# Optimization experiments

Measured on AMD Instinct MI355X. Metric: run time of the kernel, lower is better.

## Reference

```python
import jax, jax.numpy as jnp
import numpy as np

T = 2048        # q_len (current chunk)
P = 2048        # past KV cache length
HID = 4096      # hidden_size
H = 32          # num_attention_heads
D = HID // H    # head_dim = 128
THETA = 10000.0


def apply_rope(x, pos):
    # x: [H, T, D], pos: [T] int
    half = D // 2
    inv_freq = 1.0 / (THETA ** (jnp.arange(0, half, dtype=jnp.float32) / half))
    ang = pos.astype(jnp.float32)[:, None] * inv_freq[None, :]      # [T, D/2]
    cos = jnp.concatenate([jnp.cos(ang), jnp.cos(ang)], axis=-1)[None]  # [1, T, D]
    sin = jnp.concatenate([jnp.sin(ang), jnp.sin(ang)], axis=-1)[None]
    rot = jnp.concatenate([-x[..., half:], x[..., :half]], axis=-1)
    return x * cos + rot * sin


def setup_inputs() -> dict:
    key = jax.random.key(0)
    ks = jax.random.split(key, 8)
    s = 1.0 / np.sqrt(HID)
    inp = {
        "hidden_states": jax.random.normal(ks[0], (T, HID), dtype=jnp.float32),
        "attention_mask": jnp.triu(jnp.full((T, T), -jnp.inf, dtype=jnp.float32), k=1),
        "Wq": jax.random.normal(ks[1], (HID, HID), dtype=jnp.float32) * s,
        "Wk": jax.random.normal(ks[2], (HID, HID), dtype=jnp.float32) * s,
        "Wv": jax.random.normal(ks[3], (HID, HID), dtype=jnp.float32) * s,
        "Wo": jax.random.normal(ks[4], (HID, HID), dtype=jnp.float32) * s,
        "past_k": jax.random.normal(ks[5], (H, P, D), dtype=jnp.float32),
        "past_v": jax.random.normal(ks[6], (H, P, D), dtype=jnp.float32),
        "position_ids": P + jnp.arange(T, dtype=jnp.int32),
        "past_length": P,
    }
    return inp


def reference(hidden_states, attention_mask, Wq, Wk, Wv, Wo, past_k, past_v,
              position_ids, past_length):
    # QKV projections -> [H, T, D]
    proj = lambda W: (hidden_states @ W).reshape(T, H, D).transpose(1, 0, 2)
    q, k, v = proj(Wq), proj(Wk), proj(Wv)
    q = apply_rope(q, position_ids)
    k = apply_rope(k, position_ids)

    scale = 1.0 / jnp.sqrt(jnp.float32(D))
    # scores against past cache and current chunk (fp32 softmax, as in source)
    past_dots = (jnp.einsum('htd,hsd->hts', q, past_k) * scale).astype(jnp.float32)
    pmask = jnp.where(jnp.arange(P) < past_length, 0.0, -jnp.inf)  # [P]
    past_dots = past_dots + pmask
    cur = ((jnp.einsum('htd,hsd->hts', q, k) * scale) + attention_mask).astype(jnp.float32)

    # online-softmax merge via logsumexp combination
    past_lse = jax.scipy.special.logsumexp(past_dots, axis=-1, keepdims=True)
    cur_lse = jax.scipy.special.logsumexp(cur, axis=-1, keepdims=True)
    tot_lse = jnp.logaddexp(past_lse, cur_lse)
    pw = jnp.exp(past_dots - tot_lse).astype(q.dtype)
    cw = jnp.exp(cur - tot_lse).astype(q.dtype)

    out = jnp.einsum('hts,hsd->htd', pw, past_v) + jnp.einsum('hts,hsd->htd', cw, v)
    out = jnp.where(past_length == 0,
                    jnp.einsum('hts,hsd->htd', jax.nn.softmax(cur, axis=-1).astype(q.dtype), v),
                    out)
    out = out.transpose(1, 0, 2).reshape(T, HID)   # [T, hidden]
    return out @ Wo
```

## Files before the change

kernel.cpp:

```cpp
#include <hip/hip_runtime.h>
#include <cstdint>
#include <cstddef>

#define T_LEN 2048
#define PAST_MAX 2048
#define HID 4096
#define NHEAD 32
#define DHEAD 128

typedef __bf16 bf16_t;
typedef __bf16 bf16x4 __attribute__((ext_vector_type(4)));
typedef __bf16 bf16x8 __attribute__((ext_vector_type(8)));
typedef float  f32x4  __attribute__((ext_vector_type(4)));
typedef float  f32x16 __attribute__((ext_vector_type(16)));
typedef unsigned int u32x4 __attribute__((ext_vector_type(4)));

__device__ __forceinline__ void gload16(const void* g, void* l){
  __builtin_amdgcn_global_load_lds((const __attribute__((address_space(1))) void*)g,
                                   (__attribute__((address_space(3))) void*)l,
                                   16, 0, 0);
}

__device__ __forceinline__ unsigned pack_bf16(float a, float b){
  const unsigned ua = __builtin_bit_cast(unsigned short, (bf16_t)a);
  const unsigned ub = __builtin_bit_cast(unsigned short, (bf16_t)b);
  return ua | (ub << 16);
}

__global__ void cvt2_k(const float* __restrict__ a, bf16_t* __restrict__ ao,
                       const float* __restrict__ b, bf16_t* __restrict__ bo, int n4){
  int i = blockIdx.x * 256 + threadIdx.x;
  if (i < n4){
    const float4 v = ((const float4*)a)[i];
    bf16x4 o = { (bf16_t)v.x, (bf16_t)v.y, (bf16_t)v.z, (bf16_t)v.w };
    ((bf16x4*)ao)[i] = o;
  } else {
    i -= n4;
    const float4 v = ((const float4*)b)[i];
    bf16x4 o = { (bf16_t)v.x, (bf16_t)v.y, (bf16_t)v.z, (bf16_t)v.w };
    ((bf16x4*)bo)[i] = o;
  }
}

__global__ __launch_bounds__(256) void transpose2_k(const float* __restrict__ in,
                                                    bf16_t* __restrict__ out, int R, int C){
  __shared__ float tile[64][65];
  const int r0 = blockIdx.x << 6, c0 = blockIdx.y << 6;
  const size_t bo = (size_t)blockIdx.z * (size_t)R * (size_t)C;
  const int tx = threadIdx.x & 15, ty = threadIdx.x >> 4;
#pragma unroll
  for (int k = 0; k < 4; ++k){
    const float4 v = *(const float4*)(in + bo + (size_t)(r0 + ty + 16*k) * C + c0 + tx*4);
    float* tp = &tile[ty + 16*k][tx*4];
    tp[0] = v.x; tp[1] = v.y; tp[2] = v.z; tp[3] = v.w;
  }
  __syncthreads();
  const int rr0 = (threadIdx.x & 7) * 8;
  const int ccb = threadIdx.x >> 3;
#pragma unroll
  for (int k = 0; k < 2; ++k){
    const int cc = ccb + 32*k;
    bf16x8 o;
#pragma unroll
    for (int j = 0; j < 8; ++j) o[j] = (bf16_t)tile[rr0 + j][cc];
    *(bf16x8*)(out + bo + (size_t)(c0 + cc) * R + r0 + rr0) = o;
  }
}

__global__ __launch_bounds__(256) void transpose3_k(
    const float* __restrict__ s0, const float* __restrict__ s1, const float* __restrict__ s2,
    bf16_t* __restrict__ d0, bf16_t* __restrict__ d1, bf16_t* __restrict__ d2){
  __shared__ float tile[64][65];
  const float* in = (blockIdx.z == 0) ? s0 : (blockIdx.z == 1) ? s1 : s2;
  bf16_t* out = (blockIdx.z == 0) ? d0 : (blockIdx.z == 1) ? d1 : d2;
  const int r0 = blockIdx.x << 6, c0 = blockIdx.y << 6;
  const int tx = threadIdx.x & 15, ty = threadIdx.x >> 4;
#pragma unroll
  for (int k = 0; k < 4; ++k){
    const float4 v = *(const float4*)(in + (size_t)(r0 + ty + 16*k) * HID + c0 + tx*4);
    float* tp = &tile[ty + 16*k][tx*4];
    tp[0] = v.x; tp[1] = v.y; tp[2] = v.z; tp[3] = v.w;
  }
  __syncthreads();
  const int rr0 = (threadIdx.x & 7) * 8;
  const int ccb = threadIdx.x >> 3;
#pragma unroll
  for (int k = 0; k < 2; ++k){
    const int cc = ccb + 32*k;
    bf16x8 o;
#pragma unroll
    for (int j = 0; j < 8; ++j) o[j] = (bf16_t)tile[rr0 + j][cc];
    *(bf16x8*)(out + (size_t)(c0 + cc) * HID + r0 + rr0) = o;
  }
}

__global__ void ropek8_k(bf16_t* __restrict__ K, const int* __restrict__ pos){
  const int idx = blockIdx.x * 256 + threadIdx.x;
  const int jc = idx & 7;
  const int t  = (idx >> 3) & (T_LEN - 1);
  const int h  = idx >> 14;
  const size_t base = ((size_t)h * T_LEN + t) * DHEAD;
  const float p = (float)pos[t];
  bf16x8 lo = *(bf16x8*)(K + base + jc * 8);
  bf16x8 hi = *(bf16x8*)(K + base + 64 + jc * 8);
  bf16x8 olo, ohi;
#pragma unroll
  for (int j = 0; j < 8; ++j){
    const int fi = jc * 8 + j;
    const float invf = __expf(-(float)fi * 0.14391156605212898f);
    float sn, cs;
    sincosf(p * invf, &sn, &cs);
    const float b0 = (float)lo[j], b1 = (float)hi[j];
    olo[j] = (bf16_t)(b0 * cs - b1 * sn);
    ohi[j] = (bf16_t)(b1 * cs + b0 * sn);
  }
  *(bf16x8*)(K + base + jc * 8) = olo;
  *(bf16x8*)(K + base + 64 + jc * 8) = ohi;
}

#define MM6(AF, BF, PR) \
  __builtin_amdgcn_s_setprio(1); \
  _Pragma("unroll") \
  for (int kk = 0; kk < 2; ++kk){ \
    _Pragma("unroll") \
    for (int mf = 0; mf < 4; ++mf){ \
      _Pragma("unroll") \
      for (int ni = 0; ni < 2; ++ni) \
        acc[mf][(PR)*2 + ni] = __builtin_amdgcn_mfma_f32_16x16x32_bf16( \
            AF[mf][kk], BF[ni][kk], acc[mf][(PR)*2 + ni], 0, 0, 0); \
    } \
  } \
  __builtin_amdgcn_s_setprio(0); \
  __builtin_amdgcn_sched_barrier(0);

#define RDA(SET, BUF) \
  _Pragma("unroll") \
  for (int mf = 0; mf < 4; ++mf){ \
    SET[mf][0] = *(const bf16x8*)((BUF) + abase + mf * 2048 + koff0); \
    SET[mf][1] = *(const bf16x8*)((BUF) + abase + mf * 2048 + koff1); \
  }

#define RDB(SET, BUF, UOFF) \
  _Pragma("unroll") \
  for (int ni = 0; ni < 2; ++ni){ \
    SET[ni][0] = *(const bf16x8*)((BUF) + (UOFF) + bbase + ni * 2048 + koff0); \
    SET[ni][1] = *(const bf16x8*)((BUF) + (UOFF) + bbase + ni * 2048 + koff1); \
  }

#define PTOP8 \
  asm volatile("s_waitcnt vmcnt(8)" ::: "memory"); \
  __builtin_amdgcn_s_barrier(); \
  __builtin_amdgcn_sched_barrier(0);

#define PTOP0 \
  asm volatile("s_waitcnt vmcnt(0)" ::: "memory"); \
  __builtin_amdgcn_s_barrier(); \
  __builtin_amdgcn_sched_barrier(0);

#define LGK(N) \
  __builtin_amdgcn_sched_barrier(0); \
  asm volatile("s_waitcnt lgkmcnt(" #N ")" ::: "memory"); \
  __builtin_amdgcn_sched_barrier(0);

__global__ __launch_bounds__(512, 1) void gemmqkv6p_k(
    const bf16_t* __restrict__ A,
    const bf16_t* __restrict__ Bc,
    bf16_t* __restrict__ OQ, bf16_t* __restrict__ OK2, bf16_t* __restrict__ OVT)
{
  const int bid = blockIdx.x;
  const int wg  = (bid & 7) * 64 + (bid >> 3);
  const int mt  = wg & 15;
  const int nt  = wg >> 4;
  const int m0  = mt << 7;
  const int n0g = nt * 384;

  const int tid = threadIdx.x;
  const int wv = tid >> 6, lane = tid & 63, lm = lane & 15, g = lane >> 4;
  const int wr = wv >> 2, wc = wv & 3;

  __shared__ __align__(16) char smem[131072];
  char* const buf0 = smem;
  char* const buf1 = smem + 65536;

  const f32x4 fzero = {0.f, 0.f, 0.f, 0.f};
  f32x4 acc[4][6];
#pragma unroll
  for (int i = 0; i < 4; ++i)
#pragma unroll
    for (int j = 0; j < 6; ++j) acc[i][j] = fzero;

  size_t aoff[2], boff[2];
#pragma unroll
  for (int i = 0; i < 2; ++i){
    const int c = i * 512 + tid;
    const int u = c >> 3;
    const int j = ((c & 7) ^ (u & 7)) << 3;
    aoff[i] = (size_t)(m0 + u) * HID + j;
    const int bcol = (u >> 5) * 96 + (u & 31);
    boff[i] = (size_t)(n0g + bcol) * HID + j;
  }
  const int ldst0 = (wv * 64) << 4;
  const int ldst1 = (512 + wv * 64) << 4;

  auto stgA = [&](char* buf, int kt){
    if ((unsigned)kt < 64u){
      const bf16_t* src = A + (size_t)kt * 64;
      gload16(src + aoff[0], buf + ldst0);
      gload16(src + aoff[1], buf + ldst1);
    }
  };
  auto stgB = [&](char* buf, int kt, int pr){
    if ((unsigned)kt < 64u){
      const bf16_t* src = Bc + (size_t)kt * 64 + (size_t)pr * (32 * HID);
      char* dst = buf + 16384 + pr * 16384;
      gload16(src + boff[0], dst + ldst0);
      gload16(src + boff[1], dst + ldst1);
    }
  };

  const int koff0 = ((0 + g) ^ (lm & 7)) << 4;
  const int koff1 = ((4 + g) ^ (lm & 7)) << 4;
  const int abase = ((wr << 6) + lm) << 7;
  const int bbase = ((wc << 5) + lm) << 7;

  stgA(buf0, 0); stgB(buf0, 0, 0); stgB(buf0, 0, 1); stgB(buf0, 0, 2);
  stgA(buf1, 1); stgB(buf1, 1, 0); stgB(buf1, 1, 1);
  asm volatile("s_waitcnt vmcnt(6)" ::: "memory");
  __builtin_amdgcn_s_barrier();

  bf16x8 afA[4][2], afB[4][2], bU[2][2], bV[2][2];
  RDA(afA, buf0)
  RDB(bU, buf0, 16384)

  for (int i = 0; i < 31; ++i){
    const int kt0 = 2 * i;
    PTOP8
    RDB(bV, buf0, 32768)
    stgB(buf1, kt0 + 1, 2);
    LGK(4)
    MM6(afA, bU, 0)
    PTOP8
    RDB(bU, buf0, 49152)
    stgA(buf0, kt0 + 2); stgB(buf0, kt0 + 2, 0);
    LGK(4)
    MM6(afA, bV, 1)
    PTOP8
    RDA(afB, buf1)
    RDB(bV, buf1, 16384)
    stgB(buf0, kt0 + 2, 1);
    LGK(12)
    MM6(afA, bU, 2)
    PTOP8
    RDB(bU, buf1, 32768)
    stgB(buf0, kt0 + 2, 2);
    LGK(4)
    MM6(afB, bV, 0)
    PTOP8
    RDB(bV, buf1, 49152)
    stgA(buf1, kt0 + 3); stgB(buf1, kt0 + 3, 0);
    LGK(4)
    MM6(afB, bU, 1)
    PTOP8
    RDA(afA, buf0)
    RDB(bU, buf0, 16384)
    stgB(buf1, kt0 + 3, 1);
    LGK(12)
    MM6(afB, bV, 2)
  }

  PTOP0
  RDB(bV, buf0, 32768)
  stgB(buf1, 63, 2);
  LGK(4)
  MM6(afA, bU, 0)
  PTOP0
  RDB(bU, buf0, 49152)
  LGK(4)
  MM6(afA, bV, 1)
  PTOP0
  RDA(afB, buf1)
  RDB(bV, buf1, 16384)
  LGK(12)
  MM6(afA, bU, 2)
  PTOP0
  RDB(bU, buf1, 32768)
  LGK(4)
  MM6(afB, bV, 0)
  PTOP0
  RDB(bV, buf1, 49152)
  LGK(4)
  MM6(afB, bU, 1)
  LGK(0)
  MM6(afB, bV, 2)

#pragma unroll
  for (int pr = 0; pr < 3; ++pr)
#pragma unroll
    for (int ni = 0; ni < 2; ++ni){
      const int colg = n0g + wc * 96 + pr * 32 + ni * 16 + lm;
      const int z  = colg >> 12;
      const int wi = colg & 4095;
      const int hh = wi >> 7, dd = wi & 127;
      const int ai = pr * 2 + ni;
#pragma unroll
      for (int mf = 0; mf < 4; ++mf){
        const int trow0 = m0 + wr * 64 + mf * 16 + g * 4;
        if (z == 2){
          bf16x4 v4 = { (bf16_t)acc[mf][ai][0], (bf16_t)acc[mf][ai][1],
                        (bf16_t)acc[mf][ai][2], (bf16_t)acc[mf][ai][3] };
          *(bf16x4*)(OVT + ((size_t)hh * DHEAD + dd) * T_LEN + trow0) = v4;
        } else {
          bf16_t* ob = z ? OK2 : OQ;
#pragma unroll
          for (int r = 0; r < 4; ++r)
            ob[((size_t)hh * T_LEN + trow0 + r) * DHEAD + dd] = (bf16_t)acc[mf][ai][r];
        }
      }
    }
}

#define OPQUAD(PR, BF) \
  __builtin_amdgcn_s_setprio(1); \
  _Pragma("unroll") \
  for (int kk = 0; kk < 2; ++kk){ \
    _Pragma("unroll") \
    for (int mf = 0; mf < 4; ++mf){ \
      _Pragma("unroll") \
      for (int ni = 0; ni < 2; ++ni) \
        acc[mf][(PR)*2 + ni] = __builtin_amdgcn_mfma_f32_16x16x32_bf16( \
            af[mf][kk], BF[ni][kk], acc[mf][(PR)*2 + ni], 0, 0, 0); \
    } \
  } \
  __builtin_amdgcn_s_setprio(0);

__global__ __launch_bounds__(512, 1) void gemmop2p_k(
    const bf16_t* __restrict__ A, const bf16_t* __restrict__ B,
    float* __restrict__ OF)
{
  const int bid = blockIdx.x;
  const int wg  = (bid & 7) * 32 + (bid >> 3);
  const int mt  = wg & 15;
  const int nt  = wg >> 4;
  const int m0  = mt << 7;
  const int n0  = nt << 8;

  const int tid = threadIdx.x;
  const int wv = tid >> 6, lane = tid & 63, lm = lane & 15, g = lane >> 4;
  const int wr = wv >> 2, wc = wv & 3;

  __shared__ __align__(16) char smem[98304];

  const f32x4 fzero = {0.f, 0.f, 0.f, 0.f};
  f32x4 acc[4][4];
#pragma unroll
  for (int i = 0; i < 4; ++i)
#pragma unroll
    for (int j = 0; j < 4; ++j) acc[i][j] = fzero;

  size_t aoff[2], boff[2];
#pragma unroll
  for (int i = 0; i < 2; ++i){
    const int c = i * 512 + tid;
    const int u = c >> 3;
    const int j = ((c & 7) ^ (u & 7)) << 3;
    aoff[i] = (size_t)(m0 + u) * HID + j;
    const int bcol = (u >> 5) * 64 + (u & 31);
    boff[i] = (size_t)(n0 + bcol) * HID + j;
  }
  const int ldst0 = (wv * 64) << 4;
  const int ldst1 = (512 + wv * 64) << 4;

  auto stgA = [&](char* buf, int kt){
    const bf16_t* src = A + (size_t)kt * 64;
    gload16(src + aoff[0], buf + ldst0);
    gload16(src + aoff[1], buf + ldst1);
  };
  auto stgB = [&](char* buf, int kt, int pr){
    const bf16_t* src = B + (size_t)kt * 64 + (size_t)pr * (32 * HID);
    char* dst = buf + 16384 + pr * 16384;
    gload16(src + boff[0], dst + ldst0);
    gload16(src + boff[1], dst + ldst1);
  };

  const int koff0 = ((0 + g) ^ (lm & 7)) << 4;
  const int koff1 = ((4 + g) ^ (lm & 7)) << 4;
  const int abase = ((wr << 6) + lm) << 7;
  const int bbase = ((wc << 5) + lm) << 7;

  stgA(smem, 0); stgB(smem, 0, 0); stgB(smem, 0, 1);
  stgA(smem + 49152, 1); stgB(smem + 49152, 1, 0);
  asm volatile("s_waitcnt vmcnt(4)" ::: "memory");
  __builtin_amdgcn_s_barrier();

  bf16x8 af[4][2], bf[2][2];

  for (int kt = 0; kt < 64; ++kt){
    char* buf  = smem + (kt & 1) * 49152;
    char* obuf = smem + ((kt + 1) & 1) * 49152;

#pragma unroll
    for (int mf = 0; mf < 4; ++mf){
      af[mf][0] = *(const bf16x8*)(buf + abase + mf * 2048 + koff0);
      af[mf][1] = *(const bf16x8*)(buf + abase + mf * 2048 + koff1);
    }
#pragma unroll
    for (int ni = 0; ni < 2; ++ni){
      bf[ni][0] = *(const bf16x8*)(buf + 16384 + bbase + ni * 2048 + koff0);
      bf[ni][1] = *(const bf16x8*)(buf + 16384 + bbase + ni * 2048 + koff1);
    }
    if (kt + 1 < 64) stgB(obuf, kt + 1, 1);
    __builtin_amdgcn_sched_barrier(0);
    __builtin_amdgcn_s_barrier();
    asm volatile("s_waitcnt lgkmcnt(0)" ::: "memory");
    __builtin_amdgcn_sched_barrier(0);
    OPQUAD(0, bf)
    if (kt < 62) asm volatile("s_waitcnt vmcnt(6)" ::: "memory");
    else         asm volatile("s_waitcnt vmcnt(0)" ::: "memory");
    __builtin_amdgcn_sched_barrier(0);
    __builtin_amdgcn_s_barrier();

#pragma unroll
    for (int ni = 0; ni < 2; ++ni){
      bf[ni][0] = *(const bf16x8*)(buf + 32768 + bbase + ni * 2048 + koff0);
      bf[ni][1] = *(const bf16x8*)(buf + 32768 + bbase + ni * 2048 + koff1);
    }
    if (kt + 2 < 64){ stgA(buf, kt + 2); stgB(buf, kt + 2, 0); }
    __builtin_amdgcn_sched_barrier(0);
    __builtin_amdgcn_s_barrier();
    asm volatile("s_waitcnt lgkmcnt(0)" ::: "memory");
    __builtin_amdgcn_sched_barrier(0);
    OPQUAD(1, bf)
    if (kt < 62) asm volatile("s_waitcnt vmcnt(6)" ::: "memory");
    else         asm volatile("s_waitcnt vmcnt(0)" ::: "memory");
    __builtin_amdgcn_sched_barrier(0);
    __builtin_amdgcn_s_barrier();
  }

#pragma unroll
  for (int pr = 0; pr < 2; ++pr)
#pragma unroll
    for (int ni = 0; ni < 2; ++ni){
      const int col = n0 + wc * 64 + pr * 32 + ni * 16 + lm;
      const int ai = pr * 2 + ni;
#pragma unroll
      for (int mf = 0; mf < 4; ++mf)
#pragma unroll
        for (int r = 0; r < 4; ++r){
          const int trow = m0 + wr * 64 + mf * 16 + g * 4 + r;
          OF[(size_t)trow * HID + col] = acc[mf][ai][r];
        }
    }
}

__global__ __launch_bounds__(256, 2) void attn2_k(
    const bf16_t* __restrict__ Q,
    const bf16_t* __restrict__ Kc,
    const bf16_t* __restrict__ VTc,
    const bf16_t* __restrict__ Kp,
    const bf16_t* __restrict__ VTp,
    bf16_t* __restrict__ Ctx,
    const int* __restrict__ plen_p,
    const int* __restrict__ pos)
{
  const int bid = blockIdx.x;
  const int xcd = bid & 7;
  const int k   = bid >> 3;
  const int ho  = k >> 4;
  const int qraw= k & 15;
  const int h   = (xcd << 2) | ho;
  const int qb  = (ho & 2) ? (15 - qraw) : qraw;

  const int tid = threadIdx.x;
  const int w = tid >> 6, lane = tid & 63, l31 = lane & 31, hi = lane >> 5;
  const int qw0 = qb * 128 + w * 32;
  const int qrow = qw0 + l31;
  const int plen = plen_p[0];
  const int npast = (plen + 63) >> 6;
  const int NT = npast + 2 * qb + 2;

  __shared__ __align__(16) char smem[65536 + 512];
  float* lred = (float*)(smem + 65536);

  const bf16_t* qbase = Q + ((size_t)h * T_LEN + qrow) * DHEAD;
  bf16x8 qf[8];
#pragma unroll
  for (int dc = 0; dc < 8; ++dc)
    qf[dc] = *(const bf16x8*)(qbase + dc * 16 + 8 * hi);
  {
    const float ppos = (float)pos[qrow];
    const float qs = 0.08838834764831845f;
#pragma unroll
    for (int dc = 0; dc < 4; ++dc)
#pragma unroll
      for (int j = 0; j < 8; ++j){
        const int fi = dc * 16 + 8 * hi + j;
        const float invf = __expf(-(float)fi * 0.14391156605212898f);
        float sn, cs;
        sincosf(ppos * invf, &sn, &cs);
        const float a0 = (float)qf[dc][j], a1 = (float)qf[dc + 4][j];
        qf[dc][j]     = (bf16_t)((a0 * cs - a1 * sn) * qs);
        qf[dc + 4][j] = (bf16_t)((a1 * cs + a0 * sn) * qs);
      }
  }
  __builtin_amdgcn_sched_barrier(0);

  const f32x16 fz = {0.f,0.f,0.f,0.f,0.f,0.f,0.f,0.f,0.f,0.f,0.f,0.f,0.f,0.f,0.f,0.f};
  f32x16 o[4] = {fz, fz, fz, fz};
  float m = -1e30f, l = 0.f;

  auto stage = [&](int t, int buf){
    const bf16_t* kb; const bf16_t* vb;
    if (t < npast){
      const int s0 = t * 64;
      kb = Kp  + ((size_t)h * PAST_MAX + s0) * DHEAD;
      vb = VTp + (size_t)h * DHEAD * PAST_MAX + s0;
    } else {
      const int s0 = (t - npast) * 64;
      kb = Kc  + ((size_t)h * T_LEN + s0) * DHEAD;
      vb = VTc + (size_t)h * DHEAD * T_LEN + s0;
    }
    char* kl = smem + buf * 32768;
    char* vl = kl + 16384;
#pragma unroll
    for (int i = 0; i < 4; ++i){
      const int c = i * 256 + w * 64 + lane;
      const int krow = c >> 4, kcol = c & 15;
      gload16(kb + (size_t)krow * DHEAD + ((kcol ^ (krow & 7)) << 3), kl + (i * 256 + w * 64) * 16);
      const int vrow = c >> 3, vcol = c & 7;
      gload16(vb + (size_t)vrow * 2048 + ((vcol ^ (vrow & 7)) << 3), vl + (i * 256 + w * 64) * 16);
    }
  };

  stage(0, 0);
  __builtin_amdgcn_sched_barrier(0);

  for (int t = 0; t < NT; ++t){
    const int cur = t & 1;
    if (t + 1 < NT){
      stage(t + 1, cur ^ 1);
      asm volatile("s_waitcnt vmcnt(8)" ::: "memory");
    } else {
      asm volatile("s_waitcnt vmcnt(0)" ::: "memory");
    }
    __builtin_amdgcn_sched_barrier(0);
    __builtin_amdgcn_s_barrier();
    __builtin_amdgcn_sched_barrier(0);

    const bool isc = (t >= npast);
    const int s0c = (t - npast) * 64;
    const bool active = !isc || (s0c <= qw0 + 31);

    if (active){
      char* kl = smem + cur * 32768;
      char* vl = kl + 16384;

      f32x16 sacc[2] = {fz, fz};
      __builtin_amdgcn_s_setprio(1);
#pragma unroll
      for (int kvh = 0; kvh < 2; ++kvh){
        const int krow = (kvh << 5) + l31;
        const int kbo = krow << 8;
        const int sw = (krow & 7) << 4;
#pragma unroll
        for (int dc = 0; dc < 8; ++dc){
          const bf16x8 kf = *(const bf16x8*)(kl + kbo + ((dc * 32 + 16 * hi) ^ sw));
          sacc[kvh] = __builtin_amdgcn_mfma_f32_32x32x16_bf16(kf, qf[dc], sacc[kvh], 0, 0, 0);
        }
      }
      __builtin_amdgcn_s_setprio(0);

      const bool mcur  = isc && (s0c + 63 > qw0);
      const bool mpast = !isc && ((t + 1) * 64 > plen);
      float pv[2][16];
      float pm = -1e30f;
      if (mcur | mpast){
#pragma unroll
        for (int kvh = 0; kvh < 2; ++kvh)
#pragma unroll
          for (int r = 0; r < 16; ++r){
            float x = sacc[kvh][r];
            const int kvoff = (kvh << 5) + (r & 3) + 8 * (r >> 2) + 4 * hi;
            if (mcur  && (s0c + kvoff >  qrow)) x = -1e30f;
            if (mpast && (t * 64 + kvoff >= plen)) x = -1e30f;
            pv[kvh][r] = x;
            pm = fmaxf(pm, x);
          }
      } else {
#pragma unroll
        for (int kvh = 0; kvh < 2; ++kvh)
#pragma unroll
          for (int r = 0; r < 16; ++r){
            pv[kvh][r] = sacc[kvh][r];
            pm = fmaxf(pm, sacc[kvh][r]);
          }
      }
      pm = fmaxf(pm, __shfl_xor(pm, 32));

      if (!__all(pm - m <= 8.f)){
        const float mn = fmaxf(m, pm);
        const float corr = __expf(m - mn);
        m = mn;
        l *= corr;
        if (hi == 0) lred[(w << 5) + l31] = corr;
        asm volatile("s_waitcnt lgkmcnt(0)" ::: "memory");
#pragma unroll
        for (int r = 0; r < 16; ++r){
          const float cc = lred[(w << 5) + (r & 3) + 8 * (r >> 2) + 4 * hi];
#pragma unroll
          for (int nb = 0; nb < 4; ++nb) o[nb][r] *= cc;
        }
      }

      float sum = 0.f;
#pragma unroll
      for (int kvh = 0; kvh < 2; ++kvh)
#pragma unroll
        for (int r = 0; r < 16; ++r){
          const float pe = __expf(pv[kvh][r] - m);
          pv[kvh][r] = pe;
          sum += pe;
        }
      sum += __shfl_xor(sum, 32);
      l += sum;

      unsigned wds[2][8];
#pragma unroll
      for (int kvh = 0; kvh < 2; ++kvh)
#pragma unroll
        for (int i = 0; i < 8; ++i)
          wds[kvh][i] = pack_bf16(pv[kvh][2 * i], pv[kvh][2 * i + 1]);

      bf16x8 pf[4];
#pragma unroll
      for (int ks = 0; ks < 4; ++ks){
        const int s = ks & 1, kvh = ks >> 1;
        const unsigned a0 = hi ? wds[kvh][4 * s]     : wds[kvh][4 * s + 2];
        const unsigned a1 = hi ? wds[kvh][4 * s + 1] : wds[kvh][4 * s + 3];
        const unsigned z0 = (unsigned)__shfl_xor((int)a0, 32);
        const unsigned z1 = (unsigned)__shfl_xor((int)a1, 32);
        u32x4 fw;
        fw[0] = hi ? z0 : wds[kvh][4 * s];
        fw[1] = hi ? z1 : wds[kvh][4 * s + 1];
        fw[2] = hi ? wds[kvh][4 * s + 2] : z0;
        fw[3] = hi ? wds[kvh][4 * s + 3] : z1;
        pf[ks] = __builtin_bit_cast(bf16x8, fw);
      }

      __builtin_amdgcn_s_setprio(1);
#pragma unroll
      for (int ks = 0; ks < 4; ++ks)
#pragma unroll
        for (int nb = 0; nb < 4; ++nb){
          const int vrow = (nb << 5) + l31;
          const bf16x8 vf = *(const bf16x8*)(vl + (vrow << 7) + ((ks * 32 + 16 * hi) ^ ((vrow & 7) << 4)));
          o[nb] = __builtin_amdgcn_mfma_f32_32x32x16_bf16(pf[ks], vf, o[nb], 0, 0, 0);
        }
      __builtin_amdgcn_s_setprio(0);
    }
    __builtin_amdgcn_sched_barrier(0);
    __builtin_amdgcn_s_barrier();
  }

  if (hi == 0) lred[(w << 5) + l31] = l;
  asm volatile("s_waitcnt lgkmcnt(0)" ::: "memory");
#pragma unroll
  for (int r = 0; r < 16; ++r){
    const int cr = (r & 3) + 8 * (r >> 2) + 4 * hi;
    const float li = 1.f / lred[(w << 5) + cr];
    const int trow = qw0 + cr;
    bf16_t* cb = Ctx + (size_t)trow * HID + h * DHEAD + l31;
#pragma unroll
    for (int nb = 0; nb < 4; ++nb)
      cb[nb << 5] = (bf16_t)(o[nb][r] * li);
  }
}

extern "C" void kernel_launch(void* const* d_in, const int* in_sizes, int n_in,
                              void* d_out, int out_size, void* d_ws, size_t ws_size,
                              hipStream_t stream)
{
  const float* X   = (const float*)d_in[0];
  const float* Wq  = (const float*)d_in[2];
  const float* Wk  = (const float*)d_in[3];
  const float* Wv  = (const float*)d_in[4];
  const float* Wo  = (const float*)d_in[5];
  const float* PKi = (const float*)d_in[6];
  const float* PVi = (const float*)d_in[7];
  const int* POS   = (const int*)d_in[8];
  const int* PLEN  = (const int*)d_in[9];
  float* OUT = (float*)d_out;

  char* ws = (char*)d_ws;
  const size_t SZ_XB  = (size_t)T_LEN * HID * 2;
  const size_t SZ_W   = (size_t)HID * HID * 2;
  const size_t SZ_HTD = (size_t)NHEAD * T_LEN * DHEAD * 2;

  bf16_t* XB  = (bf16_t*)(ws);
  bf16_t* WT0 = (bf16_t*)(ws + SZ_XB);
  bf16_t* WT1 = (bf16_t*)(ws + SZ_XB + SZ_W);
  bf16_t* WT2 = (bf16_t*)(ws + SZ_XB + 2 * SZ_W);
  char* p = ws + SZ_XB + 3 * SZ_W;
  bf16_t* QB   = (bf16_t*)p; p += SZ_HTD;
  bf16_t* KB   = (bf16_t*)p; p += SZ_HTD;
  bf16_t* VTB  = (bf16_t*)p; p += SZ_HTD;
  bf16_t* KPB  = (bf16_t*)p; p += SZ_HTD;
  bf16_t* VPTB = (bf16_t*)p; p += SZ_HTD;
  bf16_t* CTX  = (bf16_t*)p; p += SZ_HTD;
  bf16_t* WOT  = QB;

  dim3 blk256(256);
  dim3 blk512(512);
  cvt2_k<<<16384, blk256, 0, stream>>>(X, XB, PKi, KPB, T_LEN * HID / 4);
  transpose3_k<<<dim3(64,64,3), blk256, 0, stream>>>(Wq, Wk, Wv, WT0, WT1, WT2);
  transpose2_k<<<dim3(32,2,32), blk256, 0, stream>>>(PVi, VPTB, PAST_MAX, DHEAD);

  gemmqkv6p_k<<<512, blk512, 0, stream>>>(XB, WT0, QB, KB, VTB);
  ropek8_k<<<2048, blk256, 0, stream>>>(KB, POS);
  attn2_k<<<512, blk256, 0, stream>>>(QB, KB, VTB, KPB, VPTB, CTX, PLEN, POS);

  transpose2_k<<<dim3(64,64,1), blk256, 0, stream>>>(Wo, WOT, HID, HID);
  gemmop2p_k<<<256, blk512, 0, stream>>>(CTX, WOT, OUT);
}
```

Before: 530.1 us.

## Register double-buffer output GEMM fragments and pair causal q-blocks in attention

```diff
diff --git a/kernel.cpp b/kernel.cpp
--- a/kernel.cpp
+++ b/kernel.cpp
@@ -147,13 +147,8 @@
     SET[ni][1] = *(const bf16x8*)((BUF) + (UOFF) + bbase + ni * 2048 + koff1); \
   }
 
-#define PTOP8 \
-  asm volatile("s_waitcnt vmcnt(8)" ::: "memory"); \
-  __builtin_amdgcn_s_barrier(); \
-  __builtin_amdgcn_sched_barrier(0);
-
-#define PTOP0 \
-  asm volatile("s_waitcnt vmcnt(0)" ::: "memory"); \
+#define PTOPX(N) \
+  asm volatile("s_waitcnt vmcnt(" #N ")" ::: "memory"); \
   __builtin_amdgcn_s_barrier(); \
   __builtin_amdgcn_sched_barrier(0);
 
@@ -234,33 +229,33 @@
 
   for (int i = 0; i < 31; ++i){
     const int kt0 = 2 * i;
-    PTOP8
+    PTOPX(8)
     RDB(bV, buf0, 32768)
     stgB(buf1, kt0 + 1, 2);
     LGK(4)
     MM6(afA, bU, 0)
-    PTOP8
+    PTOPX(8)
     RDB(bU, buf0, 49152)
     stgA(buf0, kt0 + 2); stgB(buf0, kt0 + 2, 0);
     LGK(4)
     MM6(afA, bV, 1)
-    PTOP8
+    PTOPX(8)
     RDA(afB, buf1)
     RDB(bV, buf1, 16384)
     stgB(buf0, kt0 + 2, 1);
     LGK(12)
     MM6(afA, bU, 2)
-    PTOP8
+    PTOPX(8)
     RDB(bU, buf1, 32768)
     stgB(buf0, kt0 + 2, 2);
     LGK(4)
     MM6(afB, bV, 0)
-    PTOP8
+    PTOPX(8)
     RDB(bV, buf1, 49152)
     stgA(buf1, kt0 + 3); stgB(buf1, kt0 + 3, 0);
     LGK(4)
     MM6(afB, bU, 1)
-    PTOP8
+    PTOPX(8)
     RDA(afA, buf0)
     RDB(bU, buf0, 16384)
     stgB(buf1, kt0 + 3, 1);
@@ -268,25 +263,25 @@
     MM6(afB, bV, 2)
   }
 
-  PTOP0
+  PTOPX(0)
   RDB(bV, buf0, 32768)
   stgB(buf1, 63, 2);
   LGK(4)
   MM6(afA, bU, 0)
-  PTOP0
+  PTOPX(0)
   RDB(bU, buf0, 49152)
   LGK(4)
   MM6(afA, bV, 1)
-  PTOP0
+  PTOPX(0)
   RDA(afB, buf1)
   RDB(bV, buf1, 16384)
   LGK(12)
   MM6(afA, bU, 2)
-  PTOP0
+  PTOPX(0)
   RDB(bU, buf1, 32768)
   LGK(4)
   MM6(afB, bV, 0)
-  PTOP0
+  PTOPX(0)
   RDB(bV, buf1, 49152)
   LGK(4)
   MM6(afB, bU, 1)
@@ -319,21 +314,7 @@
     }
 }
 
-#define OPQUAD(PR, BF) \
-  __builtin_amdgcn_s_setprio(1); \
-  _Pragma("unroll") \
-  for (int kk = 0; kk < 2; ++kk){ \
-    _Pragma("unroll") \
-    for (int mf = 0; mf < 4; ++mf){ \
-      _Pragma("unroll") \
-      for (int ni = 0; ni < 2; ++ni) \
-        acc[mf][(PR)*2 + ni] = __builtin_amdgcn_mfma_f32_16x16x32_bf16( \
-            af[mf][kk], BF[ni][kk], acc[mf][(PR)*2 + ni], 0, 0, 0); \
-    } \
-  } \
-  __builtin_amdgcn_s_setprio(0);
-
-__global__ __launch_bounds__(512, 1) void gemmop2p_k(
+__global__ __launch_bounds__(512, 1) void gemmop_ra_k(
     const bf16_t* __restrict__ A, const bf16_t* __restrict__ B,
     float* __restrict__ OF)
 {
@@ -349,6 +330,8 @@
   const int wr = wv >> 2, wc = wv & 3;
 
   __shared__ __align__(16) char smem[98304];
+  char* const buf0 = smem;
+  char* const buf1 = smem + 49152;
 
   const f32x4 fzero = {0.f, 0.f, 0.f, 0.f};
   f32x4 acc[4][4];
@@ -371,15 +354,19 @@
   const int ldst1 = (512 + wv * 64) << 4;
 
   auto stgA = [&](char* buf, int kt){
-    const bf16_t* src = A + (size_t)kt * 64;
-    gload16(src + aoff[0], buf + ldst0);
-    gload16(src + aoff[1], buf + ldst1);
+    if ((unsigned)kt < 64u){
+      const bf16_t* src = A + (size_t)kt * 64;
+      gload16(src + aoff[0], buf + ldst0);
+      gload16(src + aoff[1], buf + ldst1);
+    }
   };
   auto stgB = [&](char* buf, int kt, int pr){
-    const bf16_t* src = B + (size_t)kt * 64 + (size_t)pr * (32 * HID);
-    char* dst = buf + 16384 + pr * 16384;
-    gload16(src + boff[0], dst + ldst0);
-    gload16(src + boff[1], dst + ldst1);
+    if ((unsigned)kt < 64u){
+      const bf16_t* src = B + (size_t)kt * 64 + (size_t)pr * (32 * HID);
+      char* dst = buf + 16384 + pr * 16384;
+      gload16(src + boff[0], dst + ldst0);
+      gload16(src + boff[1], dst + ldst1);
+    }
   };
 
   const int koff0 = ((0 + g) ^ (lm & 7)) << 4;
@@ -387,54 +374,57 @@
   const int abase = ((wr << 6) + lm) << 7;
   const int bbase = ((wc << 5) + lm) << 7;
 
-  stgA(smem, 0); stgB(smem, 0, 0); stgB(smem, 0, 1);
-  stgA(smem + 49152, 1); stgB(smem + 49152, 1, 0);
+  stgA(buf0, 0); stgB(buf0, 0, 0); stgB(buf0, 0, 1);
+  stgA(buf1, 1); stgB(buf1, 1, 0);
   asm volatile("s_waitcnt vmcnt(4)" ::: "memory");
   __builtin_amdgcn_s_barrier();
 
-  bf16x8 af[4][2], bf[2][2];
-
-  for (int kt = 0; kt < 64; ++kt){
-    char* buf  = smem + (kt & 1) * 49152;
-    char* obuf = smem + ((kt + 1) & 1) * 49152;
-
-#pragma unroll
-    for (int mf = 0; mf < 4; ++mf){
-      af[mf][0] = *(const bf16x8*)(buf + abase + mf * 2048 + koff0);
-      af[mf][1] = *(const bf16x8*)(buf + abase + mf * 2048 + koff1);
-    }
-#pragma unroll
-    for (int ni = 0; ni < 2; ++ni){
-      bf[ni][0] = *(const bf16x8*)(buf + 16384 + bbase + ni * 2048 + koff0);
-      bf[ni][1] = *(const bf16x8*)(buf + 16384 + bbase + ni * 2048 + koff1);
-    }
-    if (kt + 1 < 64) stgB(obuf, kt + 1, 1);
-    __builtin_amdgcn_sched_barrier(0);
-    __builtin_amdgcn_s_barrier();
-    asm volatile("s_waitcnt lgkmcnt(0)" ::: "memory");
-    __builtin_amdgcn_sched_barrier(0);
-    OPQUAD(0, bf)
-    if (kt < 62) asm volatile("s_waitcnt vmcnt(6)" ::: "memory");
-    else         asm volatile("s_waitcnt vmcnt(0)" ::: "memory");
-    __builtin_amdgcn_sched_barrier(0);
-    __builtin_amdgcn_s_barrier();
-
-#pragma unroll
-    for (int ni = 0; ni < 2; ++ni){
-      bf[ni][0] = *(const bf16x8*)(buf + 32768 + bbase + ni * 2048 + koff0);
-      bf[ni][1] = *(const bf16x8*)(buf + 32768 + bbase + ni * 2048 + koff1);
-    }
-    if (kt + 2 < 64){ stgA(buf, kt + 2); stgB(buf, kt + 2, 0); }
-    __builtin_amdgcn_sched_barrier(0);
-    __builtin_amdgcn_s_barrier();
-    asm volatile("s_waitcnt lgkmcnt(0)" ::: "memory");
-    __builtin_amdgcn_sched_barrier(0);
-    OPQUAD(1, bf)
-    if (kt < 62) asm volatile("s_waitcnt vmcnt(6)" ::: "memory");
-    else         asm volatile("s_waitcnt vmcnt(0)" ::: "memory");
-    __builtin_amdgcn_sched_barrier(0);
-    __builtin_amdgcn_s_barrier();
-  }
+  bf16x8 afA[4][2], afB[4][2], bU[2][2], bV[2][2];
+  RDA(afA, buf0)
+  RDB(bU, buf0, 16384)
+
+  for (int i = 0; i < 31; ++i){
+    const int kt0 = 2 * i;
+    PTOPX(4)
+    RDB(bV, buf0, 32768)
+    stgB(buf1, kt0 + 1, 1);
+    LGK(4)
+    MM6(afA, bU, 0)
+    PTOPX(2)
+    RDA(afB, buf1)
+    RDB(bU, buf1, 16384)
+    stgA(buf0, kt0 + 2); stgB(buf0, kt0 + 2, 0);
+    LGK(12)
+    MM6(afA, bV, 1)
+    PTOPX(4)
+    RDB(bV, buf1, 32768)
+    stgB(buf0, kt0 + 2, 1);
+    LGK(4)
+    MM6(afB, bU, 0)
+    PTOPX(2)
+    RDA(afA, buf0)
+    RDB(bU, buf0, 16384)
+    stgA(buf1, kt0 + 3); stgB(buf1, kt0 + 3, 0);
+    LGK(12)
+    MM6(afB, bV, 1)
+  }
+
+  PTOPX(4)
+  RDB(bV, buf0, 32768)
+  stgB(buf1, 63, 1);
+  LGK(4)
+  MM6(afA, bU, 0)
+  PTOPX(2)
+  RDA(afB, buf1)
+  RDB(bU, buf1, 16384)
+  LGK(12)
+  MM6(afA, bV, 1)
+  PTOPX(0)
+  RDB(bV, buf1, 32768)
+  LGK(4)
+  MM6(afB, bU, 0)
+  LGK(0)
+  MM6(afB, bV, 1)
 
 #pragma unroll
   for (int pr = 0; pr < 2; ++pr)
@@ -465,10 +455,12 @@
   const int bid = blockIdx.x;
   const int xcd = bid & 7;
   const int k   = bid >> 3;
-  const int ho  = k >> 4;
-  const int qraw= k & 15;
+  const int p   = k >> 1;
+  const int par = k & 1;
+  const int ho  = p >> 3;
+  const int v   = p & 7;
   const int h   = (xcd << 2) | ho;
-  const int qb  = (ho & 2) ? (15 - qraw) : qraw;
+  const int qb  = par ? (15 - v) : v;
 
   const int tid = threadIdx.x;
   const int w = tid >> 6, lane = tid & 63, l31 = lane & 31, hi = lane >> 5;
@@ -719,5 +711,5 @@
   attn2_k<<<512, blk256, 0, stream>>>(QB, KB, VTB, KPB, VPTB, CTX, PLEN, POS);
 
   transpose2_k<<<dim3(64,64,1), blk256, 0, stream>>>(Wo, WOT, HID, HID);
-  gemmop2p_k<<<256, blk512, 0, stream>>>(CTX, WOT, OUT);
-}
+  gemmop_ra_k<<<256, blk512, 0, stream>>>(CTX, WOT, OUT);
+}
```

After: 536.4 us. About the same (+1.2%).
